# Kernel optimization log

Hardware: AMD Instinct MI355X
Metric: run time of the kernel (lower is better)

Reference implementation:

```python
import jax, jax.numpy as jnp
import numpy as np

B, M, N, K = 128, 32, 64, 2048  # batch, queue rows, strokes per step, stroke length (K <= M*N)


def setup_inputs() -> dict:
    key = jax.random.key(0)
    ks = jax.random.split(key, 18)
    f32 = jnp.float32
    rn = lambda k, s, sc=1.0: jax.random.normal(k, s, f32) * sc
    return {
        'qt1': rn(ks[0], (B, M, N, 2)),
        'ht1': rn(ks[1], (B, N, 2)),
        'zt': rn(ks[2], (B, N)),
        'alpha_t': jax.random.uniform(ks[3], (B, N), f32),
        'conv_w': rn(ks[4], (2, 2, M + 1, 1), 0.1),  # OIHW, kernel (M+1, 1)
        'conv_b': rn(ks[5], (2,), 0.1),
        'W_xr': rn(ks[6], (2, 2)), 'W_hr': rn(ks[7], (2, 2)), 'b_r': rn(ks[8], (2,)),
        'W_xu': rn(ks[9], (2, 2)), 'W_hu': rn(ks[10], (2, 2)), 'b_u': rn(ks[11], (2,)),
        'W_xn': rn(ks[12], (2, 2)), 'W_hn': rn(ks[13], (2, 2)), 'b_n': rn(ks[14], (2,)),
        'lin_w': rn(ks[15], (N, 2 * N), 0.05),
        'lin_b': rn(ks[16], (N,), 0.05),
        'W_emb': rn(ks[17], (K, 2), 0.1),  # stereo stroke waveform table (stands in for embedding_layer)
    }


def reference(qt1, ht1, zt, alpha_t, conv_w, conv_b, W_xr, W_hr, b_r, W_xu, W_hu, b_u, W_xn, W_hn, b_n, lin_w, lin_b, W_emb):
    Bx = qt1.shape[0]
    # memory matrix: queue + hidden state -> [B, M+1, N, 2]
    Mt1 = jnp.concatenate([qt1, ht1[:, None]], axis=1)
    # full-height (M+1,1) conv over 2 channels, position-wise over N -> [B, N, 2]
    Ht1 = jnp.einsum('bhnc,och->bno', Mt1, conv_w[..., 0]) + conv_b
    xt = jnp.stack([zt, alpha_t], axis=-1)  # [B, N, 2]
    # tiny GRU-style gating on the 2-channel state
    rt = jax.nn.sigmoid(xt @ W_xr + Ht1 @ W_hr + b_r)
    ut = jax.nn.sigmoid(xt @ W_xu + Ht1 @ W_hu + b_u)
    nt = jnp.tanh(xt @ W_xn + (rt * Ht1) @ W_hn + b_n)
    ht = ut * ht1 + (1.0 - ut) * nt  # [B, N, 2]
    it = ht.reshape(Bx, 2 * N) @ lin_w.T + lin_b  # [B, N] stroke intensities
    # embedding: intensity-scaled stroke waveform per onset -> [B, N, K, 2]
    srt = (it * alpha_t)[:, :, None, None] * W_emb[None, None]
    # shifted scatter-accumulate (overlap-add): f_srt[:, i:i+K] += srt[:, i]
    pos = (jnp.arange(N)[:, None] + jnp.arange(K)[None, :]).reshape(-1)  # [N*K]
    f_srt = jnp.zeros((Bx, N + K - 1, 2), srt.dtype).at[:, pos].add(srt.reshape(Bx, N * K, 2))
    st = qt1[:, 0] + f_srt[:, :N]  # emitted samples [B, N, 2]
    # shift queue up one row and add the remaining overlap tail into the flattened queue
    q_shift = jnp.concatenate([qt1[:, 1:], jnp.zeros_like(qt1[:, :1])], axis=1).reshape(Bx, M * N, 2)
    tail = jnp.pad(f_srt[:, N:], ((0, 0), (0, M * N - (K - 1)), (0, 0)))
    qt = (q_shift + tail).reshape(Bx, M, N, 2)
    return st, qt, ht
```

## Files before the change

kernel.cpp:

```cpp
#include <hip/hip_runtime.h>
#include <math.h>

#define NB 128
#define NM 32
#define NN 64
#define NK 2048
#define NP (NN + NK - 1)
#define NQ 4
#define QSZ 528
#define WSPAN 592

__global__ __launch_bounds__(256) void gen_cell_kernel(
    const float* __restrict__ qt1,
    const float* __restrict__ ht1,
    const float* __restrict__ zt,
    const float* __restrict__ alpha_t,
    const float* __restrict__ conv_w,
    const float* __restrict__ conv_b,
    const float* __restrict__ W_xr, const float* __restrict__ W_hr, const float* __restrict__ b_r,
    const float* __restrict__ W_xu, const float* __restrict__ W_hu, const float* __restrict__ b_u,
    const float* __restrict__ W_xn, const float* __restrict__ W_hn, const float* __restrict__ b_n,
    const float* __restrict__ lin_w, const float* __restrict__ lin_b,
    const float* __restrict__ W_emb,
    float* __restrict__ out)
{
    const int b   = blockIdx.x >> 2;
    const int q   = blockIdx.x & 3;
    const int tid = threadIdx.x;
    const int plo = q * QSZ;

    __shared__ __align__(16) float2 s_wr[WSPAN];
    __shared__ __align__(16) float s_ht[2 * NN];
    __shared__ float s_s[NN];

    {
        const float2* w2g = (const float2*)W_emb;
        const int i_min = 1584 - plo;
        float2 z2; z2.x = 0.f; z2.y = 0.f;
        for (int j = tid; j < 591; j += 256) {
            int i = i_min + j;
            float2 v = (i >= 64 && i < 2112) ? w2g[NP - i] : z2;
            s_wr[j] = v;
        }
    }

    float2* st2 = (float2*)out;
    float2* qt2 = (float2*)out + NB * NN;
    float*  ht_out = out + NB * NN * 2 + NB * NM * NN * 2;

    if (tid < NN) {
        const int n = tid;
        const float* qp = qt1 + (size_t)b * (NM * NN * 2) + n * 2;
        float h0 = conv_b[0], h1 = conv_b[1];
        #pragma unroll
        for (int h = 0; h < NM; ++h) {
            float m0 = qp[h * (NN * 2)];
            float m1 = qp[h * (NN * 2) + 1];
            h0 = fmaf(m0, conv_w[h],      fmaf(m1, conv_w[33 + h], h0));
            h1 = fmaf(m0, conv_w[66 + h], fmaf(m1, conv_w[99 + h], h1));
        }
        const float hp0 = ht1[b * (NN * 2) + n * 2];
        const float hp1 = ht1[b * (NN * 2) + n * 2 + 1];
        h0 = fmaf(hp0, conv_w[32],      fmaf(hp1, conv_w[33 + 32], h0));
        h1 = fmaf(hp0, conv_w[66 + 32], fmaf(hp1, conv_w[99 + 32], h1));

        const float x0 = zt[b * NN + n];
        const float x1 = alpha_t[b * NN + n];

        float pr0 = x0*W_xr[0] + x1*W_xr[2] + h0*W_hr[0] + h1*W_hr[2] + b_r[0];
        float pr1 = x0*W_xr[1] + x1*W_xr[3] + h0*W_hr[1] + h1*W_hr[3] + b_r[1];
        float r0 = 1.f / (1.f + expf(-pr0));
        float r1 = 1.f / (1.f + expf(-pr1));

        float pu0 = x0*W_xu[0] + x1*W_xu[2] + h0*W_hu[0] + h1*W_hu[2] + b_u[0];
        float pu1 = x0*W_xu[1] + x1*W_xu[3] + h0*W_hu[1] + h1*W_hu[3] + b_u[1];
        float u0 = 1.f / (1.f + expf(-pu0));
        float u1 = 1.f / (1.f + expf(-pu1));

        float g0 = r0 * h0, g1 = r1 * h1;
        float pn0 = x0*W_xn[0] + x1*W_xn[2] + g0*W_hn[0] + g1*W_hn[2] + b_n[0];
        float pn1 = x0*W_xn[1] + x1*W_xn[3] + g0*W_hn[1] + g1*W_hn[3] + b_n[1];
        float nt0 = tanhf(pn0);
        float nt1 = tanhf(pn1);

        float ho0 = u0 * hp0 + (1.f - u0) * nt0;
        float ho1 = u1 * hp1 + (1.f - u1) * nt1;
        s_ht[n * 2]     = ho0;
        s_ht[n * 2 + 1] = ho1;
        if (q == 0) {
            ht_out[b * (NN * 2) + n * 2]     = ho0;
            ht_out[b * (NN * 2) + n * 2 + 1] = ho1;
        }
    }
    __syncthreads();

    if (tid < NN) {
        const int n = tid;
        float acc = lin_b[n];
        const float4* lw4 = (const float4*)(lin_w + n * (2 * NN));
        const float4* h4  = (const float4*)s_ht;
        #pragma unroll
        for (int j = 0; j < 32; ++j) {
            float4 lw = lw4[j];
            float4 hv = h4[j];
            acc = fmaf(lw.x, hv.x, acc);
            acc = fmaf(lw.y, hv.y, acc);
            acc = fmaf(lw.z, hv.z, acc);
            acc = fmaf(lw.w, hv.w, acc);
        }
        s_s[n] = acc * alpha_t[b * NN + n];
    }
    __syncthreads();

    const float s_reg = s_s[tid & 63];

    const float2* q2 = (const float2*)qt1 + (size_t)b * 2048;

    {
        const float2* R0 = s_wr + (527 - tid);
        const float2* R1 = R0 - 256;
        float a00 = 0.f, a01 = 0.f, a10 = 0.f, a11 = 0.f;
        #pragma unroll 16
        for (int n = 0; n < NN; ++n) {
            float sv = __uint_as_float(
                __builtin_amdgcn_readlane(__float_as_uint(s_reg), n));
            float2 w0 = R0[n];
            float2 w1 = R1[n];
            a00 = fmaf(sv, w0.x, a00); a01 = fmaf(sv, w0.y, a01);
            a10 = fmaf(sv, w1.x, a10); a11 = fmaf(sv, w1.y, a11);
        }
        {
            const int p = plo + tid;
            float2 res; res.x = a00; res.y = a01;
            if (p < 2048) { float2 qv = q2[p]; res.x += qv.x; res.y += qv.y; }
            if (p < 64) st2[b * 64 + p] = res;
            else        qt2[(size_t)b * 2048 + p - 64] = res;
        }
        {
            const int p = plo + 256 + tid;
            float2 res; res.x = a10; res.y = a11;
            if (p < 2048) { float2 qv = q2[p]; res.x += qv.x; res.y += qv.y; }
            qt2[(size_t)b * 2048 + p - 64] = res;
        }
        if (tid < 16) {
            const int p = plo + 512 + tid;
            if (p < NP) {
                const float2* R2p = R0 - 512;
                float t0 = 0.f, t1 = 0.f;
                #pragma unroll 16
                for (int n = 0; n < NN; ++n) {
                    float sv = __uint_as_float(
                        __builtin_amdgcn_readlane(__float_as_uint(s_reg), n));
                    float2 wv = R2p[n];
                    t0 = fmaf(sv, wv.x, t0);
                    t1 = fmaf(sv, wv.y, t1);
                }
                float2 res; res.x = t0; res.y = t1;
                if (p < 2048) { float2 qv = q2[p]; res.x += qv.x; res.y += qv.y; }
                qt2[(size_t)b * 2048 + p - 64] = res;
            }
        }
    }

    if (q == 3 && tid == 0) {
        float2 z; z.x = 0.f; z.y = 0.f;
        qt2[(size_t)b * 2048 + 2047] = z;
    }
}

extern "C" void kernel_launch(void* const* d_in, const int* in_sizes, int n_in,
                              void* d_out, int out_size, void* d_ws, size_t ws_size,
                              hipStream_t stream) {
    (void)in_sizes; (void)n_in; (void)out_size; (void)d_ws; (void)ws_size;
    gen_cell_kernel<<<dim3(NB * NQ), dim3(256), 0, stream>>>(
        (const float*)d_in[0],  (const float*)d_in[1],  (const float*)d_in[2],
        (const float*)d_in[3],  (const float*)d_in[4],  (const float*)d_in[5],
        (const float*)d_in[6],  (const float*)d_in[7],  (const float*)d_in[8],
        (const float*)d_in[9],  (const float*)d_in[10], (const float*)d_in[11],
        (const float*)d_in[12], (const float*)d_in[13], (const float*)d_in[14],
        (const float*)d_in[15], (const float*)d_in[16], (const float*)d_in[17],
        (float*)d_out);
}
```

Before: 100.9 us.

## Prefetch queue loads early, split GEMV and tail across lanes, use fast math

The queue values the outputs need are now loaded at kernel start, so their global latency overlaps the weight staging and GRU math. The GRU uses fast sigmoid and tanh built on hardware exp and reciprocal. The conv reduction splits into two accumulator chains. The 64x128 linear layer is spread over all 256 threads with shuffle reductions, and the tail positions use a 4-lane split instead of 16 serial lanes. The accumulators use packed two-wide vector types so the compiler can emit packed FMAs. Fast math slightly changes accuracy, and the early loads keep more registers live.

```diff
diff --git a/kernel.cpp b/kernel.cpp
--- a/kernel.cpp
+++ b/kernel.cpp
@@ -9,6 +9,15 @@
 #define NQ 4
 #define QSZ 528
 #define WSPAN 592
+
+typedef float v2f __attribute__((ext_vector_type(2)));
+
+__device__ __forceinline__ float fast_sigmoid(float x) {
+    return __builtin_amdgcn_rcpf(1.f + __expf(-x));
+}
+__device__ __forceinline__ float fast_tanh(float x) {
+    return 1.f - 2.f * __builtin_amdgcn_rcpf(1.f + __expf(2.f * x));
+}
 
 __global__ __launch_bounds__(256) void gen_cell_kernel(
     const float* __restrict__ qt1,
@@ -33,6 +42,19 @@
     __shared__ __align__(16) float s_ht[2 * NN];
     __shared__ float s_s[NN];
 
+    const float2* q2 = (const float2*)qt1 + (size_t)b * 2048;
+
+    const int p0 = plo + tid;
+    const int p1 = p0 + 256;
+    float2 qv0 = q2[p0];
+    float2 qv1; qv1.x = 0.f; qv1.y = 0.f;
+    if (p1 < 2048) qv1 = q2[p1];
+    float2 qv2; qv2.x = 0.f; qv2.y = 0.f;
+    if (tid >= 64 && tid < 128) {
+        const int pt = plo + 512 + ((tid - 64) >> 2);
+        if (pt < 2048) qv2 = q2[pt];
+    }
+
     {
         const float2* w2g = (const float2*)W_emb;
         const int i_min = 1584 - plo;
@@ -51,37 +73,43 @@
     if (tid < NN) {
         const int n = tid;
         const float* qp = qt1 + (size_t)b * (NM * NN * 2) + n * 2;
-        float h0 = conv_b[0], h1 = conv_b[1];
+        float h0a = 0.f, h0b = 0.f, h1a = 0.f, h1b = 0.f;
         #pragma unroll
-        for (int h = 0; h < NM; ++h) {
+        for (int h = 0; h < NM; h += 2) {
             float m0 = qp[h * (NN * 2)];
             float m1 = qp[h * (NN * 2) + 1];
-            h0 = fmaf(m0, conv_w[h],      fmaf(m1, conv_w[33 + h], h0));
-            h1 = fmaf(m0, conv_w[66 + h], fmaf(m1, conv_w[99 + h], h1));
+            float m2 = qp[(h + 1) * (NN * 2)];
+            float m3 = qp[(h + 1) * (NN * 2) + 1];
+            h0a = fmaf(m0, conv_w[h],       fmaf(m1, conv_w[33 + h],  h0a));
+            h0b = fmaf(m2, conv_w[h + 1],   fmaf(m3, conv_w[34 + h],  h0b));
+            h1a = fmaf(m0, conv_w[66 + h],  fmaf(m1, conv_w[99 + h],  h1a));
+            h1b = fmaf(m2, conv_w[67 + h],  fmaf(m3, conv_w[100 + h], h1b));
         }
         const float hp0 = ht1[b * (NN * 2) + n * 2];
         const float hp1 = ht1[b * (NN * 2) + n * 2 + 1];
-        h0 = fmaf(hp0, conv_w[32],      fmaf(hp1, conv_w[33 + 32], h0));
-        h1 = fmaf(hp0, conv_w[66 + 32], fmaf(hp1, conv_w[99 + 32], h1));
+        float h0 = h0a + h0b + conv_b[0];
+        float h1 = h1a + h1b + conv_b[1];
+        h0 = fmaf(hp0, conv_w[32], fmaf(hp1, conv_w[65],  h0));
+        h1 = fmaf(hp0, conv_w[98], fmaf(hp1, conv_w[131], h1));
 
         const float x0 = zt[b * NN + n];
         const float x1 = alpha_t[b * NN + n];
 
         float pr0 = x0*W_xr[0] + x1*W_xr[2] + h0*W_hr[0] + h1*W_hr[2] + b_r[0];
         float pr1 = x0*W_xr[1] + x1*W_xr[3] + h0*W_hr[1] + h1*W_hr[3] + b_r[1];
-        float r0 = 1.f / (1.f + expf(-pr0));
-        float r1 = 1.f / (1.f + expf(-pr1));
+        float r0 = fast_sigmoid(pr0);
+        float r1 = fast_sigmoid(pr1);
 
         float pu0 = x0*W_xu[0] + x1*W_xu[2] + h0*W_hu[0] + h1*W_hu[2] + b_u[0];
         float pu1 = x0*W_xu[1] + x1*W_xu[3] + h0*W_hu[1] + h1*W_hu[3] + b_u[1];
-        float u0 = 1.f / (1.f + expf(-pu0));
-        float u1 = 1.f / (1.f + expf(-pu1));
+        float u0 = fast_sigmoid(pu0);
+        float u1 = fast_sigmoid(pu1);
 
         float g0 = r0 * h0, g1 = r1 * h1;
         float pn0 = x0*W_xn[0] + x1*W_xn[2] + g0*W_hn[0] + g1*W_hn[2] + b_n[0];
         float pn1 = x0*W_xn[1] + x1*W_xn[3] + g0*W_hn[1] + g1*W_hn[3] + b_n[1];
-        float nt0 = tanhf(pn0);
-        float nt1 = tanhf(pn1);
+        float nt0 = fast_tanh(pn0);
+        float nt1 = fast_tanh(pn1);
 
         float ho0 = u0 * hp0 + (1.f - u0) * nt0;
         float ho1 = u1 * hp1 + (1.f - u1) * nt1;
@@ -94,13 +122,15 @@
     }
     __syncthreads();
 
-    if (tid < NN) {
-        const int n = tid;
-        float acc = lin_b[n];
+    {
+        const int n   = tid >> 2;
+        const int sub = tid & 3;
         const float4* lw4 = (const float4*)(lin_w + n * (2 * NN));
         const float4* h4  = (const float4*)s_ht;
+        float acc = 0.f;
         #pragma unroll
-        for (int j = 0; j < 32; ++j) {
+        for (int jj = 0; jj < 8; ++jj) {
+            const int j = sub + 4 * jj;
             float4 lw = lw4[j];
             float4 hv = h4[j];
             acc = fmaf(lw.x, hv.x, acc);
@@ -108,57 +138,59 @@
             acc = fmaf(lw.z, hv.z, acc);
             acc = fmaf(lw.w, hv.w, acc);
         }
-        s_s[n] = acc * alpha_t[b * NN + n];
+        acc += __shfl_xor(acc, 1);
+        acc += __shfl_xor(acc, 2);
+        if (sub == 0) s_s[n] = (acc + lin_b[n]) * alpha_t[b * NN + n];
     }
     __syncthreads();
 
     const float s_reg = s_s[tid & 63];
-
-    const float2* q2 = (const float2*)qt1 + (size_t)b * 2048;
 
     {
         const float2* R0 = s_wr + (527 - tid);
         const float2* R1 = R0 - 256;
-        float a00 = 0.f, a01 = 0.f, a10 = 0.f, a11 = 0.f;
+        v2f a0 = {0.f, 0.f};
+        v2f a1 = {0.f, 0.f};
         #pragma unroll 16
         for (int n = 0; n < NN; ++n) {
             float sv = __uint_as_float(
                 __builtin_amdgcn_readlane(__float_as_uint(s_reg), n));
-            float2 w0 = R0[n];
-            float2 w1 = R1[n];
-            a00 = fmaf(sv, w0.x, a00); a01 = fmaf(sv, w0.y, a01);
-            a10 = fmaf(sv, w1.x, a10); a11 = fmaf(sv, w1.y, a11);
+            v2f w0 = *(const v2f*)(R0 + n);
+            v2f w1 = *(const v2f*)(R1 + n);
+            a0 += w0 * sv;
+            a1 += w1 * sv;
         }
         {
-            const int p = plo + tid;
-            float2 res; res.x = a00; res.y = a01;
-            if (p < 2048) { float2 qv = q2[p]; res.x += qv.x; res.y += qv.y; }
-            if (p < 64) st2[b * 64 + p] = res;
-            else        qt2[(size_t)b * 2048 + p - 64] = res;
+            float2 res; res.x = a0.x + qv0.x; res.y = a0.y + qv0.y;
+            if (p0 < 64) st2[b * 64 + p0] = res;
+            else         qt2[(size_t)b * 2048 + p0 - 64] = res;
         }
         {
-            const int p = plo + 256 + tid;
-            float2 res; res.x = a10; res.y = a11;
-            if (p < 2048) { float2 qv = q2[p]; res.x += qv.x; res.y += qv.y; }
+            float2 res; res.x = a1.x + qv1.x; res.y = a1.y + qv1.y;
+            qt2[(size_t)b * 2048 + p1 - 64] = res;
+        }
+    }
+
+    if (tid >= 64 && tid < 128) {
+        const int l   = tid - 64;
+        const int i   = l >> 2;
+        const int sub = l & 3;
+        const int p   = plo + 512 + i;
+        const float2* Rt = s_wr + (15 - i + sub);
+        v2f acc = {0.f, 0.f};
+        #pragma unroll
+        for (int j = 0; j < 16; ++j) {
+            float sv = s_s[sub + 4 * j];
+            v2f wv = *(const v2f*)(Rt + 4 * j);
+            acc += wv * sv;
+        }
+        acc.x += __shfl_xor(acc.x, 1);
+        acc.y += __shfl_xor(acc.y, 1);
+        acc.x += __shfl_xor(acc.x, 2);
+        acc.y += __shfl_xor(acc.y, 2);
+        if (sub == 0 && p < NP) {
+            float2 res; res.x = acc.x + qv2.x; res.y = acc.y + qv2.y;
             qt2[(size_t)b * 2048 + p - 64] = res;
-        }
-        if (tid < 16) {
-            const int p = plo + 512 + tid;
-            if (p < NP) {
-                const float2* R2p = R0 - 512;
-                float t0 = 0.f, t1 = 0.f;
-                #pragma unroll 16
-                for (int n = 0; n < NN; ++n) {
-                    float sv = __uint_as_float(
-                        __builtin_amdgcn_readlane(__float_as_uint(s_reg), n));
-                    float2 wv = R2p[n];
-                    t0 = fmaf(sv, wv.x, t0);
-                    t1 = fmaf(sv, wv.y, t1);
-                }
-                float2 res; res.x = t0; res.y = t1;
-                if (p < 2048) { float2 qv = q2[p]; res.x += qv.x; res.y += qv.y; }
-                qt2[(size_t)b * 2048 + p - 64] = res;
-            }
         }
     }
 
```

Result: faster. 98.51 us (-2.4%).
